# Kernel tuning notes

Measured on AMD Instinct MI355X. Metric: run time of the kernel, lower is better.

## Reference

```python
import jax, jax.numpy as jnp
import numpy as np

B, S, D = 16, 1024, 768

def setup_inputs() -> dict:
    key = jax.random.key(0)
    k1, k2, k3, k4 = jax.random.split(key, 4)
    head = jax.random.normal(k1, (B, S, D), dtype=jnp.float32)
    dep = jax.random.normal(k2, (B, S, D), dtype=jnp.float32)
    edge_W = jax.random.normal(k3, (1, 2 * D), dtype=jnp.float32)
    edge_b = jax.random.normal(k4, (1,), dtype=jnp.float32)
    return {"head": head, "dep": dep, "edge_W": edge_W, "edge_b": edge_b}

def reference(head, dep, edge_W, edge_b):
    # Original: scores[b,i,j] = edge_W @ concat(head[b,i], dep[b,j]) + edge_b
    # Separable: split W into head-half and dep-half, broadcast-add over grid.
    d = head.shape[-1]
    w_h = edge_W[0, :d]   # [D]
    w_d = edge_W[0, d:]   # [D]
    s_h = jnp.einsum('bid,d->bi', head, w_h)  # [B,S]
    s_d = jnp.einsum('bjd,d->bj', dep, w_d)   # [B,S]
    return s_h[:, :, None] + s_d[:, None, :] + edge_b[0]  # [B,S,S]
```

## Files before the change

kernel.cpp:

```cpp
#include <hip/hip_runtime.h>
#include <hip/hip_bf16.h>


#define B_SZ 16
#define S_SZ 1024
#define D_SZ 768

__global__ __launch_bounds__(256) void dot_rows_kernel(
    const float* __restrict__ head,
    const float* __restrict__ dep,
    const float* __restrict__ edge_W,
    float* __restrict__ s_out)
{
    const int rows = B_SZ * S_SZ;
    const int wave = (blockIdx.x * blockDim.x + threadIdx.x) >> 6;
    const int lane = threadIdx.x & 63;
    if (wave >= 2 * rows) return;

    const float* src;
    const float* w;
    int row;
    if (wave < rows) { src = head; w = edge_W;         row = wave; }
    else             { src = dep;  w = edge_W + D_SZ;  row = wave - rows; }

    const float4* __restrict__ p  =
        reinterpret_cast<const float4*>(src + (size_t)row * D_SZ);
    const float4* __restrict__ wp = reinterpret_cast<const float4*>(w);

    float acc = 0.f;
#pragma unroll
    for (int k = 0; k < 3; ++k) {
        float4 a = p[lane + k * 64];
        float4 b = wp[lane + k * 64];
        acc += a.x * b.x + a.y * b.y + a.z * b.z + a.w * b.w;
    }
#pragma unroll
    for (int off = 32; off > 0; off >>= 1)
        acc += __shfl_down(acc, off, 64);

    if (lane == 0) s_out[wave] = acc;
}

__global__ __launch_bounds__(256) void bcast_kernel(
    const float* __restrict__ s_h,
    const float* __restrict__ s_d,
    const float* __restrict__ edge_b,
    float* __restrict__ out)
{
    const int row = blockIdx.x;
    const int b   = row >> 10;
    const int t   = threadIdx.x;

    const float base = s_h[row] + edge_b[0];
    float4 sd = reinterpret_cast<const float4*>(s_d + ((size_t)b << 10))[t];

    float4 o;
    o.x = base + sd.x;
    o.y = base + sd.y;
    o.z = base + sd.z;
    o.w = base + sd.w;
    reinterpret_cast<float4*>(out + ((size_t)row << 10))[t] = o;
}

extern "C" void kernel_launch(void* const* d_in, const int* in_sizes, int n_in,
                              void* d_out, int out_size, void* d_ws, size_t ws_size,
                              hipStream_t stream) {
    const float* head   = (const float*)d_in[0];
    const float* dep    = (const float*)d_in[1];
    const float* edge_W = (const float*)d_in[2];
    const float* edge_b = (const float*)d_in[3];
    float* out = (float*)d_out;

    float* s = (float*)d_ws;
    const int rows = B_SZ * S_SZ;

    {
        int total_waves = 2 * rows;
        int blocks = (total_waves * 64 + 255) / 256;
        dot_rows_kernel<<<blocks, 256, 0, stream>>>(head, dep, edge_W, s);
    }

    {
        bcast_kernel<<<rows, 256, 0, stream>>>(s, s + rows, edge_b, out);
    }
}
```

Measured before the change: 31.83 us.

## Fuse row-dot and broadcast kernels into one cooperative persistent kernel

```diff
diff --git a/kernel.cpp b/kernel.cpp
--- a/kernel.cpp
+++ b/kernel.cpp
@@ -1,65 +1,78 @@
 #include <hip/hip_runtime.h>
 #include <hip/hip_bf16.h>
+#include <hip/hip_cooperative_groups.h>
+
+namespace cg = cooperative_groups;
 
 
 #define B_SZ 16
 #define S_SZ 1024
 #define D_SZ 768
+#define NBLOCKS 1024
+#define NTHREADS 256
+#define ROWS (B_SZ * S_SZ)
+#define ROWS_PER_BLOCK (ROWS / NBLOCKS)
 
-__global__ __launch_bounds__(256) void dot_rows_kernel(
+typedef float fx4 __attribute__((ext_vector_type(4)));
+
+__global__ __launch_bounds__(NTHREADS, 4) void fused_affine_edge_kernel(
     const float* __restrict__ head,
     const float* __restrict__ dep,
     const float* __restrict__ edge_W,
-    float* __restrict__ s_out)
-{
-    const int rows = B_SZ * S_SZ;
-    const int wave = (blockIdx.x * blockDim.x + threadIdx.x) >> 6;
-    const int lane = threadIdx.x & 63;
-    if (wave >= 2 * rows) return;
-
-    const float* src;
-    const float* w;
-    int row;
-    if (wave < rows) { src = head; w = edge_W;         row = wave; }
-    else             { src = dep;  w = edge_W + D_SZ;  row = wave - rows; }
-
-    const float4* __restrict__ p  =
-        reinterpret_cast<const float4*>(src + (size_t)row * D_SZ);
-    const float4* __restrict__ wp = reinterpret_cast<const float4*>(w);
-
-    float acc = 0.f;
-#pragma unroll
-    for (int k = 0; k < 3; ++k) {
-        float4 a = p[lane + k * 64];
-        float4 b = wp[lane + k * 64];
-        acc += a.x * b.x + a.y * b.y + a.z * b.z + a.w * b.w;
-    }
-#pragma unroll
-    for (int off = 32; off > 0; off >>= 1)
-        acc += __shfl_down(acc, off, 64);
-
-    if (lane == 0) s_out[wave] = acc;
-}
-
-__global__ __launch_bounds__(256) void bcast_kernel(
-    const float* __restrict__ s_h,
-    const float* __restrict__ s_d,
     const float* __restrict__ edge_b,
+    float* __restrict__ s,
     float* __restrict__ out)
 {
-    const int row = blockIdx.x;
-    const int b   = row >> 10;
-    const int t   = threadIdx.x;
+    const int lane   = threadIdx.x & 63;
+    const int wid    = (blockIdx.x * NTHREADS + threadIdx.x) >> 6;
+    const int nwaves = (NBLOCKS * NTHREADS) >> 6;
 
-    const float base = s_h[row] + edge_b[0];
-    float4 sd = reinterpret_cast<const float4*>(s_d + ((size_t)b << 10))[t];
+    const fx4* __restrict__ wp = reinterpret_cast<const fx4*>(edge_W);
+    for (int r = wid; r < 2 * ROWS; r += nwaves) {
+        const float* src;
+        const fx4* wvec;
+        int row;
+        if (r < ROWS) { src = head; wvec = wp;              row = r; }
+        else          { src = dep;  wvec = wp + (D_SZ / 4); row = r - ROWS; }
 
-    float4 o;
-    o.x = base + sd.x;
-    o.y = base + sd.y;
-    o.z = base + sd.z;
-    o.w = base + sd.w;
-    reinterpret_cast<float4*>(out + ((size_t)row << 10))[t] = o;
+        const fx4* __restrict__ p =
+            reinterpret_cast<const fx4*>(src + (size_t)row * D_SZ);
+        float acc = 0.f;
+#pragma unroll
+        for (int k = 0; k < 3; ++k) {
+            fx4 a = __builtin_nontemporal_load(&p[lane + k * 64]);
+            fx4 b = wvec[lane + k * 64];
+            acc += a.x * b.x + a.y * b.y + a.z * b.z + a.w * b.w;
+        }
+#pragma unroll
+        for (int off = 32; off > 0; off >>= 1)
+            acc += __shfl_down(acc, off, 64);
+        if (lane == 0) s[r] = acc;
+    }
+
+    cg::this_grid().sync();
+
+    const float bias = edge_b[0];
+    const float* __restrict__ s_h = s;
+    const float* __restrict__ s_d = s + ROWS;
+
+    const int row0 = blockIdx.x * ROWS_PER_BLOCK;
+    const int b    = row0 >> 10;
+
+    fx4 sd = reinterpret_cast<const fx4*>(s_d + ((size_t)b << 10))[threadIdx.x];
+    sd.x += bias; sd.y += bias; sd.z += bias; sd.w += bias;
+
+#pragma unroll
+    for (int k = 0; k < ROWS_PER_BLOCK; ++k) {
+        const float sh = s_h[row0 + k];
+        fx4 o;
+        o.x = sh + sd.x;
+        o.y = sh + sd.y;
+        o.z = sh + sd.z;
+        o.w = sh + sd.w;
+        fx4* dst = reinterpret_cast<fx4*>(out + ((size_t)(row0 + k) << 10));
+        __builtin_nontemporal_store(o, &dst[threadIdx.x]);
+    }
 }
 
 extern "C" void kernel_launch(void* const* d_in, const int* in_sizes, int n_in,
@@ -70,17 +83,10 @@
     const float* edge_W = (const float*)d_in[2];
     const float* edge_b = (const float*)d_in[3];
     float* out = (float*)d_out;
+    float* s   = (float*)d_ws;
 
-    float* s = (float*)d_ws;
-    const int rows = B_SZ * S_SZ;
-
-    {
-        int total_waves = 2 * rows;
-        int blocks = (total_waves * 64 + 255) / 256;
-        dot_rows_kernel<<<blocks, 256, 0, stream>>>(head, dep, edge_W, s);
-    }
-
-    {
-        bcast_kernel<<<rows, 256, 0, stream>>>(s, s + rows, edge_b, out);
-    }
+    void* args[] = { (void*)&head, (void*)&dep, (void*)&edge_W, (void*)&edge_b,
+                     (void*)&s, (void*)&out };
+    (void)hipLaunchCooperativeKernel((void*)fused_affine_edge_kernel,
+                                     dim3(NBLOCKS), dim3(NTHREADS), args, 0, stream);
 }
```

New measurement: 120.0 us. 3.77x slower.
